# Performance work log

Hardware: AMD Instinct MI355X
Metric: run time of the kernel (lower is better)

The kernel has to match this reference:

```python
import jax, jax.numpy as jnp
import numpy as np

B, L, E, H = 8, 1024, 768, 12
D = E // H  # 64 head dim


def _layernorm(x, scale, bias, eps=1e-6):
    m = jnp.mean(x, axis=-1, keepdims=True)
    v = jnp.var(x, axis=-1, keepdims=True)
    return (x - m) * jax.lax.rsqrt(v + eps) * scale + bias


def setup_inputs() -> dict:
    key = jax.random.key(0)
    ks = jax.random.split(key, 8)
    s = lambda fan_in: 1.0 / np.sqrt(fan_in)  # lecun-normal-ish init scale
    return {
        "x": jax.random.normal(ks[0], (B, L, E), jnp.float32),
        "ln1_scale": jnp.ones((E,), jnp.float32),
        "ln1_bias": jnp.zeros((E,), jnp.float32),
        "w_qkv": jax.random.normal(ks[1], (E, 3 * E), jnp.float32) * s(E),
        "b_qkv": jnp.zeros((3 * E,), jnp.float32),
        "w_proj": jax.random.normal(ks[2], (E, E), jnp.float32) * s(E),
        "b_proj": jnp.zeros((E,), jnp.float32),
        "ln2_scale": jnp.ones((E,), jnp.float32),
        "ln2_bias": jnp.zeros((E,), jnp.float32),
        "w_fc": jax.random.normal(ks[3], (E, 4 * E), jnp.float32) * s(E),
        "b_fc": jnp.zeros((4 * E,), jnp.float32),
        "w_out": jax.random.normal(ks[4], (4 * E, E), jnp.float32) * s(4 * E),
        "b_out": jnp.zeros((E,), jnp.float32),
    }


def reference(x, ln1_scale, ln1_bias, w_qkv, b_qkv, w_proj, b_proj,
              ln2_scale, ln2_bias, w_fc, b_fc, w_out, b_out):
    # eval mode: train=False (all dropouts are identity), mask_len=None
    b, l, _ = x.shape
    # ---- pre-LN causal self-attention ----
    z = _layernorm(x, ln1_scale, ln1_bias)
    qkv = z @ w_qkv + b_qkv                                   # (B, L, 3E)
    # faithful to source: reshape to (B, L, H, 3D) then split last axis
    qkv = qkv.reshape(b, l, H, 3 * D).transpose(0, 2, 1, 3)   # (B, H, L, 3D)
    q, k, v = jnp.split(qkv, 3, axis=-1)                      # each (B, H, L, D)
    attn = jnp.einsum("bhqd,bhkd->bhqk", q, k) / jnp.sqrt(jnp.float32(D))
    mask = jnp.tri(l, dtype=jnp.float32)                      # causal lower-tri
    attn = jnp.where(mask == 0, -1e18, attn)
    attn = jax.nn.softmax(attn, axis=-1)
    y = jnp.einsum("bhqk,bhkd->bhqd", attn, v)                # (B, H, L, D)
    y = y.transpose(0, 2, 1, 3).reshape(b, l, E)
    y = y @ w_proj + b_proj
    x = x + y  # residual (resid dropout is identity in eval)
    # ---- MLP block ----
    z = _layernorm(x, ln2_scale, ln2_bias)
    z = jax.nn.selu(z @ w_fc + b_fc) @ w_out + b_out
    return x + z
```

## Files before the change

kernel.cpp:

```cpp
#include <hip/hip_runtime.h>
#include <hip/hip_bf16.h>

typedef __attribute__((ext_vector_type(8))) short short8;
typedef __attribute__((ext_vector_type(4))) float f32x4;
typedef __attribute__((ext_vector_type(4))) unsigned short us4;

#define AS1 __attribute__((address_space(1)))
#define AS3 __attribute__((address_space(3)))

__device__ __forceinline__ unsigned short f2bf(float f) {
    unsigned u = __float_as_uint(f);
    u += 0x7fffu + ((u >> 16) & 1u);
    return (unsigned short)(u >> 16);
}

__device__ __forceinline__ void gload16(const void* g, void* l) {
    __builtin_amdgcn_global_load_lds((AS1 void*)(g), (AS3 void*)(l), 16, 0, 0);
}

__global__ __launch_bounds__(256) void wT_kernel(const float* __restrict__ in,
                                                 unsigned short* __restrict__ out,
                                                 int K, int N) {
    __shared__ float tile[32][33];
    int tx = threadIdx.x & 31, ty = threadIdx.x >> 5;
    int bn = blockIdx.x * 32, bk = blockIdx.y * 32;
    #pragma unroll
    for (int i = ty; i < 32; i += 8)
        tile[i][tx] = in[(long)(bk + i) * N + bn + tx];
    __syncthreads();
    #pragma unroll
    for (int i = ty; i < 32; i += 8)
        out[(long)(bn + i) * K + bk + tx] = f2bf(tile[tx][i]);
}

__global__ __launch_bounds__(256) void ln_row(const float* __restrict__ x,
                                              const float* __restrict__ sc,
                                              const float* __restrict__ bi,
                                              unsigned short* __restrict__ z) {
    long row = blockIdx.x;
    const float* xr = x + row * 768;
    int t = threadIdx.x;
    float v0 = xr[t], v1 = xr[t + 256], v2 = xr[t + 512];
    float s = v0 + v1 + v2;
    float ss = v0 * v0 + v1 * v1 + v2 * v2;
    #pragma unroll
    for (int m = 1; m < 64; m <<= 1) { s += __shfl_xor(s, m); ss += __shfl_xor(ss, m); }
    __shared__ float red[8];
    int wid = t >> 6;
    if ((t & 63) == 0) { red[wid] = s; red[4 + wid] = ss; }
    __syncthreads();
    s = red[0] + red[1] + red[2] + red[3];
    ss = red[4] + red[5] + red[6] + red[7];
    float mean = s * (1.f / 768.f);
    float var = fmaxf(ss * (1.f / 768.f) - mean * mean, 0.f);
    float rs = rsqrtf(var + 1e-6f);
    unsigned short* zr = z + row * 768;
    zr[t]       = f2bf((v0 - mean) * rs * sc[t]       + bi[t]);
    zr[t + 256] = f2bf((v1 - mean) * rs * sc[t + 256] + bi[t + 256]);
    zr[t + 512] = f2bf((v2 - mean) * rs * sc[t + 512] + bi[t + 512]);
}

template <int MODE>
__global__ __launch_bounds__(256, 2) void gemm_bf16(
    const unsigned short* __restrict__ A, const unsigned short* __restrict__ Bt,
    const float* __restrict__ bias, const float* __restrict__ resid,
    float* __restrict__ outf, unsigned short* __restrict__ outb,
    unsigned short* __restrict__ vt, int M, int N, int K) {
    __shared__ unsigned short As[128 * 64];
    __shared__ unsigned short Bs[128 * 64];
    const int tid = threadIdx.x, lane = tid & 63, wid = tid >> 6;
    const int wr = wid >> 1, wc = wid & 1;
    const long row0 = (long)blockIdx.y * 128, col0 = (long)blockIdx.x * 128;

    f32x4 acc[4][4] = {};
    const int nkt = K >> 6;
    for (int t = 0; t < nkt; ++t) {
        #pragma unroll
        for (int kq = 0; kq < 4; kq++) {
            int U = kq * 256 + tid;
            int r = U >> 3, ch = U & 7;
            int kb = (ch * 16) ^ ((r & 7) << 4);
            gload16(A + (row0 + r) * K + t * 64 + (kb >> 1), &As[(kq * 256 + wid * 64) * 8]);
            gload16(Bt + (col0 + r) * K + t * 64 + (kb >> 1), &Bs[(kq * 256 + wid * 64) * 8]);
        }
        __syncthreads();
        #pragma unroll
        for (int kk = 0; kk < 2; kk++) {
            short8 af[4], bf[4];
            #pragma unroll
            for (int m = 0; m < 4; m++) {
                int r = wr * 64 + m * 16 + (lane & 15);
                int off = r * 128 + ((kk * 64 + ((lane >> 4) * 16)) ^ ((r & 7) << 4));
                af[m] = *(const short8*)((const char*)As + off);
            }
            #pragma unroll
            for (int n = 0; n < 4; n++) {
                int r = wc * 64 + n * 16 + (lane & 15);
                int off = r * 128 + ((kk * 64 + ((lane >> 4) * 16)) ^ ((r & 7) << 4));
                bf[n] = *(const short8*)((const char*)Bs + off);
            }
            #pragma unroll
            for (int m = 0; m < 4; m++)
                #pragma unroll
                for (int n = 0; n < 4; n++)
                    acc[m][n] = __builtin_amdgcn_mfma_f32_16x16x32_bf16(af[m], bf[n], acc[m][n], 0, 0, 0);
        }
        __syncthreads();
    }

    const float LAM = 1.0507009873554805f, LAMAL = 1.7580993408473766f;
    #pragma unroll
    for (int n = 0; n < 4; n++) {
        int c = (int)col0 + wc * 64 + n * 16 + (lane & 15);
        float bv = bias[c];
        #pragma unroll
        for (int m = 0; m < 4; m++) {
            long r0 = row0 + wr * 64 + m * 16 + ((lane >> 4) * 4);
            f32x4 v = acc[m][n];
            v += bv;
            if (MODE == 0) {
                int h = c / 192, rem = c - h * 192;
                if (rem < 128) {
                    #pragma unroll
                    for (int r = 0; r < 4; r++) outb[(r0 + r) * 2304 + c] = f2bf(v[r]);
                } else {
                    int d = rem - 128;
                    long bb = r0 >> 10, l = r0 & 1023;
                    us4 p;
                    #pragma unroll
                    for (int r = 0; r < 4; r++) p[r] = f2bf(v[r]);
                    *(us4*)(vt + ((bb * 12 + h) * 64 + d) * 1024 + l) = p;
                }
            } else if (MODE == 1) {
                #pragma unroll
                for (int r = 0; r < 4; r++)
                    outf[(r0 + r) * (long)N + c] = v[r] + resid[(r0 + r) * (long)N + c];
            } else if (MODE == 2) {
                #pragma unroll
                for (int r = 0; r < 4; r++) {
                    float s = v[r];
                    s = s > 0.f ? LAM * s : LAMAL * (__expf(s) - 1.f);
                    outb[(r0 + r) * (long)N + c] = f2bf(s);
                }
            }
        }
    }
}

__global__ __launch_bounds__(256, 2) void attn_kernel(const unsigned short* __restrict__ qkv,
                                                      const unsigned short* __restrict__ vt,
                                                      unsigned short* __restrict__ y) {
    __shared__ unsigned short Qs[128 * 64];
    __shared__ unsigned short Ks[64 * 64];
    __shared__ unsigned short Vs[64 * 64];
    __shared__ unsigned short Ps[4][32 * 64];
    const int tid = threadIdx.x, lane = tid & 63, wid = tid >> 6;
    const int bh = blockIdx.x, qt = blockIdx.y;
    const int b = bh / 12, h = bh - b * 12;
    const long qrow0 = (long)b * 1024 + qt * 128;

    const unsigned short* qptr = qkv + qrow0 * 2304 + h * 192;
    #pragma unroll
    for (int kq = 0; kq < 4; kq++) {
        int U = kq * 256 + tid;
        int r = U >> 3, ch = U & 7;
        int kb = (ch * 16) ^ ((r & 7) << 4);
        gload16(qptr + (long)r * 2304 + (kb >> 1), &Qs[(kq * 256 + wid * 64) * 8]);
    }
    __syncthreads();
    short8 qf[2][2];
    #pragma unroll
    for (int m = 0; m < 2; m++)
        #pragma unroll
        for (int kk = 0; kk < 2; kk++) {
            int r = wid * 32 + m * 16 + (lane & 15);
            int off = r * 128 + ((kk * 64 + ((lane >> 4) * 16)) ^ ((r & 7) << 4));
            qf[m][kk] = *(const short8*)((const char*)Qs + off);
        }

    f32x4 O[2][4] = {};
    float mrow[2][4], lrow[2][4];
    #pragma unroll
    for (int m = 0; m < 2; m++)
        #pragma unroll
        for (int r = 0; r < 4; r++) { mrow[m][r] = -3.0e38f; lrow[m][r] = 0.f; }

    const int qlo = qt * 128 + wid * 32;
    const int nkv = (qt + 1) * 2;
    const unsigned short* kptr = qkv + (long)b * 1024 * 2304 + h * 192 + 64;
    const unsigned short* vptr = vt + (long)bh * 64 * 1024;

    for (int kvt = 0; kvt < nkv; ++kvt) {
        #pragma unroll
        for (int kq = 0; kq < 2; kq++) {
            int U = kq * 256 + tid;
            int r = U >> 3, ch = U & 7;
            int kb = (ch * 16) ^ ((r & 7) << 4);
            gload16(kptr + (long)(kvt * 64 + r) * 2304 + (kb >> 1), &Ks[(kq * 256 + wid * 64) * 8]);
            gload16(vptr + (long)r * 1024 + kvt * 64 + (kb >> 1), &Vs[(kq * 256 + wid * 64) * 8]);
        }
        __syncthreads();
        if (kvt * 64 <= qlo + 31) {
            f32x4 s[2][4] = {};
            #pragma unroll
            for (int kk = 0; kk < 2; kk++) {
                short8 kf[4];
                #pragma unroll
                for (int n = 0; n < 4; n++) {
                    int r = n * 16 + (lane & 15);
                    int off = r * 128 + ((kk * 64 + ((lane >> 4) * 16)) ^ ((r & 7) << 4));
                    kf[n] = *(const short8*)((const char*)Ks + off);
                }
                #pragma unroll
                for (int m = 0; m < 2; m++)
                    #pragma unroll
                    for (int n = 0; n < 4; n++)
                        s[m][n] = __builtin_amdgcn_mfma_f32_16x16x32_bf16(qf[m][kk], kf[n], s[m][n], 0, 0, 0);
            }
            const bool needmask = (kvt * 64 + 63) > qlo;
            #pragma unroll
            for (int m = 0; m < 2; m++)
                #pragma unroll
                for (int n = 0; n < 4; n++) {
                    s[m][n] = s[m][n] * 0.125f;
                    if (needmask) {
                        int c = kvt * 64 + n * 16 + (lane & 15);
                        #pragma unroll
                        for (int r = 0; r < 4; r++) {
                            int rr = qlo + m * 16 + ((lane >> 4) * 4) + r;
                            if (c > rr) s[m][n][r] = -1.0e30f;
                        }
                    }
                }
            #pragma unroll
            for (int m = 0; m < 2; m++)
                #pragma unroll
                for (int r = 0; r < 4; r++) {
                    float mx = fmaxf(fmaxf(s[m][0][r], s[m][1][r]), fmaxf(s[m][2][r], s[m][3][r]));
                    #pragma unroll
                    for (int msk = 1; msk < 16; msk <<= 1) mx = fmaxf(mx, __shfl_xor(mx, msk));
                    float mnew = fmaxf(mrow[m][r], mx);
                    float al = __expf(mrow[m][r] - mnew);
                    float ps = 0.f;
                    #pragma unroll
                    for (int n = 0; n < 4; n++) {
                        float p = __expf(s[m][n][r] - mnew);
                        s[m][n][r] = p;
                        ps += p;
                    }
                    #pragma unroll
                    for (int msk = 1; msk < 16; msk <<= 1) ps += __shfl_xor(ps, msk);
                    lrow[m][r] = lrow[m][r] * al + ps;
                    mrow[m][r] = mnew;
                    #pragma unroll
                    for (int n = 0; n < 4; n++) O[m][n][r] *= al;
                }
            unsigned short* pw = Ps[wid];
            #pragma unroll
            for (int m = 0; m < 2; m++)
                #pragma unroll
                for (int n = 0; n < 4; n++)
                    #pragma unroll
                    for (int r = 0; r < 4; r++) {
                        int pr = m * 16 + ((lane >> 4) * 4) + r;
                        int off = (pr * 128 + (n * 16 + (lane & 15)) * 2) ^ ((pr & 7) << 4);
                        *(unsigned short*)((char*)pw + off) = f2bf(s[m][n][r]);
                    }
            #pragma unroll
            for (int kk = 0; kk < 2; kk++) {
                short8 pf[2], vf[4];
                #pragma unroll
                for (int m = 0; m < 2; m++) {
                    int r = m * 16 + (lane & 15);
                    int off = r * 128 + ((kk * 64 + ((lane >> 4) * 16)) ^ ((r & 7) << 4));
                    pf[m] = *(const short8*)((const char*)pw + off);
                }
                #pragma unroll
                for (int n = 0; n < 4; n++) {
                    int r = n * 16 + (lane & 15);
                    int off = r * 128 + ((kk * 64 + ((lane >> 4) * 16)) ^ ((r & 7) << 4));
                    vf[n] = *(const short8*)((const char*)Vs + off);
                }
                #pragma unroll
                for (int m = 0; m < 2; m++)
                    #pragma unroll
                    for (int n = 0; n < 4; n++)
                        O[m][n] = __builtin_amdgcn_mfma_f32_16x16x32_bf16(pf[m], vf[n], O[m][n], 0, 0, 0);
            }
        }
        __syncthreads();
    }
    unsigned short* yb = y + (qrow0 + wid * 32) * 768 + h * 64;
    #pragma unroll
    for (int m = 0; m < 2; m++)
        #pragma unroll
        for (int n = 0; n < 4; n++)
            #pragma unroll
            for (int r = 0; r < 4; r++) {
                int rr = m * 16 + ((lane >> 4) * 4) + r;
                yb[(long)rr * 768 + n * 16 + (lane & 15)] = f2bf(O[m][n][r] / lrow[m][r]);
            }
}

extern "C" void kernel_launch(void* const* d_in, const int* in_sizes, int n_in,
                              void* d_out, int out_size, void* d_ws, size_t ws_size,
                              hipStream_t stream) {
    (void)in_sizes; (void)n_in; (void)out_size; (void)ws_size;
    const float* x      = (const float*)d_in[0];
    const float* ln1_s  = (const float*)d_in[1];
    const float* ln1_b  = (const float*)d_in[2];
    const float* w_qkv  = (const float*)d_in[3];
    const float* b_qkv  = (const float*)d_in[4];
    const float* w_proj = (const float*)d_in[5];
    const float* b_proj = (const float*)d_in[6];
    const float* ln2_s  = (const float*)d_in[7];
    const float* ln2_b  = (const float*)d_in[8];
    const float* w_fc   = (const float*)d_in[9];
    const float* b_fc   = (const float*)d_in[10];
    const float* w_out  = (const float*)d_in[11];
    const float* b_out  = (const float*)d_in[12];

    unsigned short* wqkvT = (unsigned short*)d_ws;
    unsigned short* wprojT = wqkvT + (size_t)2304 * 768;
    unsigned short* wfcT   = wprojT + (size_t)768 * 768;
    unsigned short* woutT  = wfcT + (size_t)3072 * 768;
    unsigned short* zbuf   = woutT + (size_t)768 * 3072;
    unsigned short* qkvb   = zbuf + (size_t)8192 * 768;
    unsigned short* vtb    = qkvb + (size_t)8192 * 2304;
    unsigned short* abuf   = qkvb;
    float* x2 = (float*)(vtb + (size_t)96 * 64 * 1024);

    wT_kernel<<<dim3(72, 24), 256, 0, stream>>>(w_qkv, wqkvT, 768, 2304);
    wT_kernel<<<dim3(24, 24), 256, 0, stream>>>(w_proj, wprojT, 768, 768);
    wT_kernel<<<dim3(96, 24), 256, 0, stream>>>(w_fc, wfcT, 768, 3072);
    wT_kernel<<<dim3(24, 96), 256, 0, stream>>>(w_out, woutT, 3072, 768);

    ln_row<<<8192, 256, 0, stream>>>(x, ln1_s, ln1_b, zbuf);
    gemm_bf16<0><<<dim3(18, 64), 256, 0, stream>>>(zbuf, wqkvT, b_qkv, nullptr, nullptr, qkvb, vtb, 8192, 2304, 768);
    attn_kernel<<<dim3(96, 8), 256, 0, stream>>>(qkvb, vtb, zbuf);
    gemm_bf16<1><<<dim3(6, 64), 256, 0, stream>>>(zbuf, wprojT, b_proj, x, x2, nullptr, nullptr, 8192, 768, 768);
    ln_row<<<8192, 256, 0, stream>>>(x2, ln2_s, ln2_b, zbuf);
    gemm_bf16<2><<<dim3(24, 64), 256, 0, stream>>>(zbuf, wfcT, b_fc, nullptr, nullptr, abuf, nullptr, 8192, 3072, 768);
    gemm_bf16<1><<<dim3(6, 64), 256, 0, stream>>>(abuf, woutT, b_out, x2, (float*)d_out, nullptr, nullptr, 8192, 768, 3072);
}
```

Before: 423.2 us.

## Add double-buffered 256x256 GEMM and pair causal attention tiles per block

Adds a 512-thread GEMM kernel with 256x256 tiles that double-buffers LDS, prefetches the next K tile in two halves between MFMA phases, and raises wave priority around MFMA runs. It is used for the QKV and FC projections. The attention kernel now handles two query tiles per block (qt and 7-qt), which evens out the causal work per block and halves the grid. The cost is 128KB of LDS per block and more registers, which may limit occupancy, and a smaller grid for both kernels.

```diff
diff --git a/kernel.cpp b/kernel.cpp
--- a/kernel.cpp
+++ b/kernel.cpp
@@ -7,6 +7,9 @@
 
 #define AS1 __attribute__((address_space(1)))
 #define AS3 __attribute__((address_space(3)))
+
+#define BARRIER() asm volatile("s_barrier" ::: "memory")
+#define WAITV0()  asm volatile("s_waitcnt vmcnt(0)" ::: "memory")
 
 __device__ __forceinline__ unsigned short f2bf(float f) {
     unsigned u = __float_as_uint(f);
@@ -61,6 +64,153 @@
 }
 
 template <int MODE>
+__global__ __launch_bounds__(512, 2) void gemm256(
+    const unsigned short* __restrict__ A, const unsigned short* __restrict__ Bt,
+    const float* __restrict__ bias,
+    float* __restrict__ outf, unsigned short* __restrict__ outb,
+    unsigned short* __restrict__ vt, int M, int N, int K) {
+    __shared__ unsigned short As[2][256 * 64];
+    __shared__ unsigned short Bs[2][256 * 64];
+    const int tid = threadIdx.x, lane = tid & 63, wid = tid >> 6;
+    const int wm = wid >> 2, wn = wid & 3;
+    const long row0 = (long)blockIdx.y * 256, col0 = (long)blockIdx.x * 256;
+    const int nkt = K >> 6;
+
+    auto stgA = [&](int buf, int t, int h) {
+        #pragma unroll
+        for (int j = 0; j < 2; j++) {
+            int U = j * 512 + tid;
+            int r = (U >> 3) + h * 128, ch = U & 7;
+            int kb = (ch * 16) ^ ((r & 7) << 4);
+            gload16(A + (row0 + r) * K + (long)t * 64 + (kb >> 1), &As[buf][(h * 1024 + U) * 8]);
+        }
+    };
+    auto stgB = [&](int buf, int t, int h) {
+        #pragma unroll
+        for (int j = 0; j < 2; j++) {
+            int U = j * 512 + tid;
+            int r = (U >> 3) + h * 128, ch = U & 7;
+            int kb = (ch * 16) ^ ((r & 7) << 4);
+            gload16(Bt + (col0 + r) * K + (long)t * 64 + (kb >> 1), &Bs[buf][(h * 1024 + U) * 8]);
+        }
+    };
+    auto rdA = [&](int buf, int m, int kk) -> short8 {
+        int r = wm * 128 + m * 16 + (lane & 15);
+        int off = r * 128 + ((kk * 64 + ((lane >> 4) * 16)) ^ ((r & 7) << 4));
+        return *(const short8*)((const char*)&As[buf][0] + off);
+    };
+    auto rdB = [&](int buf, int n, int kk) -> short8 {
+        int r = wn * 64 + n * 16 + (lane & 15);
+        int off = r * 128 + ((kk * 64 + ((lane >> 4) * 16)) ^ ((r & 7) << 4));
+        return *(const short8*)((const char*)&Bs[buf][0] + off);
+    };
+
+    f32x4 acc[8][4] = {};
+    stgA(0, 0, 0); stgB(0, 0, 0); stgA(0, 0, 1); stgB(0, 0, 1);
+    WAITV0();
+    BARRIER();
+
+    short8 a4[4][2], bl[2][2], bh[2][2];
+    for (int t = 0; t < nkt; ++t) {
+        const int cur = t & 1, nxt = cur ^ 1;
+        const bool pf = (t + 1 < nkt);
+        if (pf) { stgA(nxt, t + 1, 0); stgB(nxt, t + 1, 0); }
+        #pragma unroll
+        for (int m = 0; m < 4; m++) { a4[m][0] = rdA(cur, m, 0); a4[m][1] = rdA(cur, m, 1); }
+        #pragma unroll
+        for (int n = 0; n < 2; n++) { bl[n][0] = rdB(cur, n, 0); bl[n][1] = rdB(cur, n, 1); }
+        BARRIER();
+        __builtin_amdgcn_s_setprio(1);
+        #pragma unroll
+        for (int m = 0; m < 4; m++)
+            #pragma unroll
+            for (int n = 0; n < 2; n++)
+                #pragma unroll
+                for (int kk = 0; kk < 2; kk++)
+                    acc[m][n] = __builtin_amdgcn_mfma_f32_16x16x32_bf16(a4[m][kk], bl[n][kk], acc[m][n], 0, 0, 0);
+        __builtin_amdgcn_s_setprio(0);
+        BARRIER();
+        if (pf) { stgA(nxt, t + 1, 1); stgB(nxt, t + 1, 1); }
+        #pragma unroll
+        for (int n = 0; n < 2; n++) { bh[n][0] = rdB(cur, n + 2, 0); bh[n][1] = rdB(cur, n + 2, 1); }
+        BARRIER();
+        __builtin_amdgcn_s_setprio(1);
+        #pragma unroll
+        for (int m = 0; m < 4; m++)
+            #pragma unroll
+            for (int n = 0; n < 2; n++)
+                #pragma unroll
+                for (int kk = 0; kk < 2; kk++)
+                    acc[m][n + 2] = __builtin_amdgcn_mfma_f32_16x16x32_bf16(a4[m][kk], bh[n][kk], acc[m][n + 2], 0, 0, 0);
+        __builtin_amdgcn_s_setprio(0);
+        BARRIER();
+        #pragma unroll
+        for (int m = 0; m < 4; m++) { a4[m][0] = rdA(cur, m + 4, 0); a4[m][1] = rdA(cur, m + 4, 1); }
+        BARRIER();
+        __builtin_amdgcn_s_setprio(1);
+        #pragma unroll
+        for (int m = 0; m < 4; m++)
+            #pragma unroll
+            for (int n = 0; n < 2; n++)
+                #pragma unroll
+                for (int kk = 0; kk < 2; kk++)
+                    acc[m + 4][n + 2] = __builtin_amdgcn_mfma_f32_16x16x32_bf16(a4[m][kk], bh[n][kk], acc[m + 4][n + 2], 0, 0, 0);
+        __builtin_amdgcn_s_setprio(0);
+        BARRIER();
+        WAITV0();
+        BARRIER();
+        __builtin_amdgcn_s_setprio(1);
+        #pragma unroll
+        for (int m = 0; m < 4; m++)
+            #pragma unroll
+            for (int n = 0; n < 2; n++)
+                #pragma unroll
+                for (int kk = 0; kk < 2; kk++)
+                    acc[m + 4][n] = __builtin_amdgcn_mfma_f32_16x16x32_bf16(a4[m][kk], bl[n][kk], acc[m + 4][n], 0, 0, 0);
+        __builtin_amdgcn_s_setprio(0);
+        BARRIER();
+    }
+
+    const float LAM = 1.0507009873554805f, LAMAL = 1.7580993408473766f;
+    #pragma unroll
+    for (int n = 0; n < 4; n++) {
+        int c = (int)col0 + wn * 64 + n * 16 + (lane & 15);
+        float bv = bias[c];
+        #pragma unroll
+        for (int m = 0; m < 8; m++) {
+            long r0 = row0 + wm * 128 + m * 16 + ((lane >> 4) * 4);
+            f32x4 v = acc[m][n];
+            v += bv;
+            if (MODE == 0) {
+                int h = c / 192, rem = c - h * 192;
+                if (rem < 128) {
+                    #pragma unroll
+                    for (int r = 0; r < 4; r++) outb[(r0 + r) * 2304 + c] = f2bf(v[r]);
+                } else {
+                    int d = rem - 128;
+                    long bb = r0 >> 10, l = r0 & 1023;
+                    us4 p;
+                    #pragma unroll
+                    for (int r = 0; r < 4; r++) p[r] = f2bf(v[r]);
+                    *(us4*)(vt + ((bb * 12 + h) * 64 + d) * 1024 + l) = p;
+                }
+            } else if (MODE == 2) {
+                #pragma unroll
+                for (int r = 0; r < 4; r++) {
+                    float s = v[r];
+                    s = s > 0.f ? LAM * s : LAMAL * (__expf(s) - 1.f);
+                    outb[(r0 + r) * (long)N + c] = f2bf(s);
+                }
+            } else {
+                #pragma unroll
+                for (int r = 0; r < 4; r++)
+                    outf[(r0 + r) * (long)N + c] = v[r];
+            }
+        }
+    }
+}
+
+template <int MODE>
 __global__ __launch_bounds__(256, 2) void gemm_bf16(
     const unsigned short* __restrict__ A, const unsigned short* __restrict__ Bt,
     const float* __restrict__ bias, const float* __restrict__ resid,
@@ -108,7 +258,6 @@
         __syncthreads();
     }
 
-    const float LAM = 1.0507009873554805f, LAMAL = 1.7580993408473766f;
     #pragma unroll
     for (int n = 0; n < 4; n++) {
         int c = (int)col0 + wc * 64 + n * 16 + (lane & 15);
@@ -118,31 +267,9 @@
             long r0 = row0 + wr * 64 + m * 16 + ((lane >> 4) * 4);
             f32x4 v = acc[m][n];
             v += bv;
-            if (MODE == 0) {
-                int h = c / 192, rem = c - h * 192;
-                if (rem < 128) {
-                    #pragma unroll
-                    for (int r = 0; r < 4; r++) outb[(r0 + r) * 2304 + c] = f2bf(v[r]);
-                } else {
-                    int d = rem - 128;
-                    long bb = r0 >> 10, l = r0 & 1023;
-                    us4 p;
-                    #pragma unroll
-                    for (int r = 0; r < 4; r++) p[r] = f2bf(v[r]);
-                    *(us4*)(vt + ((bb * 12 + h) * 64 + d) * 1024 + l) = p;
-                }
-            } else if (MODE == 1) {
-                #pragma unroll
-                for (int r = 0; r < 4; r++)
-                    outf[(r0 + r) * (long)N + c] = v[r] + resid[(r0 + r) * (long)N + c];
-            } else if (MODE == 2) {
-                #pragma unroll
-                for (int r = 0; r < 4; r++) {
-                    float s = v[r];
-                    s = s > 0.f ? LAM * s : LAMAL * (__expf(s) - 1.f);
-                    outb[(r0 + r) * (long)N + c] = f2bf(s);
-                }
-            }
+            #pragma unroll
+            for (int r = 0; r < 4; r++)
+                outf[(r0 + r) * (long)N + c] = v[r] + resid[(r0 + r) * (long)N + c];
         }
     }
 }
@@ -155,151 +282,156 @@
     __shared__ unsigned short Vs[64 * 64];
     __shared__ unsigned short Ps[4][32 * 64];
     const int tid = threadIdx.x, lane = tid & 63, wid = tid >> 6;
-    const int bh = blockIdx.x, qt = blockIdx.y;
+    const int bh = blockIdx.x;
     const int b = bh / 12, h = bh - b * 12;
-    const long qrow0 = (long)b * 1024 + qt * 128;
-
-    const unsigned short* qptr = qkv + qrow0 * 2304 + h * 192;
-    #pragma unroll
-    for (int kq = 0; kq < 4; kq++) {
-        int U = kq * 256 + tid;
-        int r = U >> 3, ch = U & 7;
-        int kb = (ch * 16) ^ ((r & 7) << 4);
-        gload16(qptr + (long)r * 2304 + (kb >> 1), &Qs[(kq * 256 + wid * 64) * 8]);
-    }
-    __syncthreads();
-    short8 qf[2][2];
-    #pragma unroll
-    for (int m = 0; m < 2; m++)
-        #pragma unroll
-        for (int kk = 0; kk < 2; kk++) {
-            int r = wid * 32 + m * 16 + (lane & 15);
-            int off = r * 128 + ((kk * 64 + ((lane >> 4) * 16)) ^ ((r & 7) << 4));
-            qf[m][kk] = *(const short8*)((const char*)Qs + off);
-        }
-
-    f32x4 O[2][4] = {};
-    float mrow[2][4], lrow[2][4];
-    #pragma unroll
-    for (int m = 0; m < 2; m++)
-        #pragma unroll
-        for (int r = 0; r < 4; r++) { mrow[m][r] = -3.0e38f; lrow[m][r] = 0.f; }
-
-    const int qlo = qt * 128 + wid * 32;
-    const int nkv = (qt + 1) * 2;
     const unsigned short* kptr = qkv + (long)b * 1024 * 2304 + h * 192 + 64;
     const unsigned short* vptr = vt + (long)bh * 64 * 1024;
 
-    for (int kvt = 0; kvt < nkv; ++kvt) {
-        #pragma unroll
-        for (int kq = 0; kq < 2; kq++) {
+    #pragma unroll
+    for (int qi = 0; qi < 2; qi++) {
+        const int qt = qi ? (7 - (int)blockIdx.y) : (int)blockIdx.y;
+        const long qrow0 = (long)b * 1024 + qt * 128;
+
+        const unsigned short* qptr = qkv + qrow0 * 2304 + h * 192;
+        #pragma unroll
+        for (int kq = 0; kq < 4; kq++) {
             int U = kq * 256 + tid;
             int r = U >> 3, ch = U & 7;
             int kb = (ch * 16) ^ ((r & 7) << 4);
-            gload16(kptr + (long)(kvt * 64 + r) * 2304 + (kb >> 1), &Ks[(kq * 256 + wid * 64) * 8]);
-            gload16(vptr + (long)r * 1024 + kvt * 64 + (kb >> 1), &Vs[(kq * 256 + wid * 64) * 8]);
+            gload16(qptr + (long)r * 2304 + (kb >> 1), &Qs[(kq * 256 + wid * 64) * 8]);
         }
         __syncthreads();
-        if (kvt * 64 <= qlo + 31) {
-            f32x4 s[2][4] = {};
+        short8 qf[2][2];
+        #pragma unroll
+        for (int m = 0; m < 2; m++)
             #pragma unroll
             for (int kk = 0; kk < 2; kk++) {
-                short8 kf[4];
-                #pragma unroll
-                for (int n = 0; n < 4; n++) {
-                    int r = n * 16 + (lane & 15);
-                    int off = r * 128 + ((kk * 64 + ((lane >> 4) * 16)) ^ ((r & 7) << 4));
-                    kf[n] = *(const short8*)((const char*)Ks + off);
+                int r = wid * 32 + m * 16 + (lane & 15);
+                int off = r * 128 + ((kk * 64 + ((lane >> 4) * 16)) ^ ((r & 7) << 4));
+                qf[m][kk] = *(const short8*)((const char*)Qs + off);
+            }
+
+        f32x4 O[2][4] = {};
+        float mrow[2][4], lrow[2][4];
+        #pragma unroll
+        for (int m = 0; m < 2; m++)
+            #pragma unroll
+            for (int r = 0; r < 4; r++) { mrow[m][r] = -3.0e38f; lrow[m][r] = 0.f; }
+
+        const int qlo = qt * 128 + wid * 32;
+        const int nkv = (qt + 1) * 2;
+
+        for (int kvt = 0; kvt < nkv; ++kvt) {
+            #pragma unroll
+            for (int kq = 0; kq < 2; kq++) {
+                int U = kq * 256 + tid;
+                int r = U >> 3, ch = U & 7;
+                int kb = (ch * 16) ^ ((r & 7) << 4);
+                gload16(kptr + (long)(kvt * 64 + r) * 2304 + (kb >> 1), &Ks[(kq * 256 + wid * 64) * 8]);
+                gload16(vptr + (long)r * 1024 + kvt * 64 + (kb >> 1), &Vs[(kq * 256 + wid * 64) * 8]);
+            }
+            __syncthreads();
+            if (kvt * 64 <= qlo + 31) {
+                f32x4 s[2][4] = {};
+                #pragma unroll
+                for (int kk = 0; kk < 2; kk++) {
+                    short8 kf[4];
+                    #pragma unroll
+                    for (int n = 0; n < 4; n++) {
+                        int r = n * 16 + (lane & 15);
+                        int off = r * 128 + ((kk * 64 + ((lane >> 4) * 16)) ^ ((r & 7) << 4));
+                        kf[n] = *(const short8*)((const char*)Ks + off);
+                    }
+                    #pragma unroll
+                    for (int m = 0; m < 2; m++)
+                        #pragma unroll
+                        for (int n = 0; n < 4; n++)
+                            s[m][n] = __builtin_amdgcn_mfma_f32_16x16x32_bf16(qf[m][kk], kf[n], s[m][n], 0, 0, 0);
                 }
+                const bool needmask = (kvt * 64 + 63) > qlo;
                 #pragma unroll
                 for (int m = 0; m < 2; m++)
                     #pragma unroll
-                    for (int n = 0; n < 4; n++)
-                        s[m][n] = __builtin_amdgcn_mfma_f32_16x16x32_bf16(qf[m][kk], kf[n], s[m][n], 0, 0, 0);
-            }
-            const bool needmask = (kvt * 64 + 63) > qlo;
-            #pragma unroll
-            for (int m = 0; m < 2; m++)
-                #pragma unroll
-                for (int n = 0; n < 4; n++) {
-                    s[m][n] = s[m][n] * 0.125f;
-                    if (needmask) {
-                        int c = kvt * 64 + n * 16 + (lane & 15);
-                        #pragma unroll
-                        for (int r = 0; r < 4; r++) {
-                            int rr = qlo + m * 16 + ((lane >> 4) * 4) + r;
-                            if (c > rr) s[m][n][r] = -1.0e30f;
+                    for (int n = 0; n < 4; n++) {
+                        s[m][n] = s[m][n] * 0.125f;
+                        if (needmask) {
+                            int c = kvt * 64 + n * 16 + (lane & 15);
+                            #pragma unroll
+                            for (int r = 0; r < 4; r++) {
+                                int rr = qlo + m * 16 + ((lane >> 4) * 4) + r;
+                                if (c > rr) s[m][n][r] = -1.0e30f;
+                            }
                         }
                     }
+                #pragma unroll
+                for (int m = 0; m < 2; m++)
+                    #pragma unroll
+                    for (int r = 0; r < 4; r++) {
+                        float mx = fmaxf(fmaxf(s[m][0][r], s[m][1][r]), fmaxf(s[m][2][r], s[m][3][r]));
+                        #pragma unroll
+                        for (int msk = 1; msk < 16; msk <<= 1) mx = fmaxf(mx, __shfl_xor(mx, msk));
+                        float mnew = fmaxf(mrow[m][r], mx);
+                        float al = __expf(mrow[m][r] - mnew);
+                        float ps = 0.f;
+                        #pragma unroll
+                        for (int n = 0; n < 4; n++) {
+                            float p = __expf(s[m][n][r] - mnew);
+                            s[m][n][r] = p;
+                            ps += p;
+                        }
+                        #pragma unroll
+                        for (int msk = 1; msk < 16; msk <<= 1) ps += __shfl_xor(ps, msk);
+                        lrow[m][r] = lrow[m][r] * al + ps;
+                        mrow[m][r] = mnew;
+                        #pragma unroll
+                        for (int n = 0; n < 4; n++) O[m][n][r] *= al;
+                    }
+                unsigned short* pw = Ps[wid];
+                #pragma unroll
+                for (int m = 0; m < 2; m++)
+                    #pragma unroll
+                    for (int n = 0; n < 4; n++)
+                        #pragma unroll
+                        for (int r = 0; r < 4; r++) {
+                            int pr = m * 16 + ((lane >> 4) * 4) + r;
+                            int off = (pr * 128 + (n * 16 + (lane & 15)) * 2) ^ ((pr & 7) << 4);
+                            *(unsigned short*)((char*)pw + off) = f2bf(s[m][n][r]);
+                        }
+                #pragma unroll
+                for (int kk = 0; kk < 2; kk++) {
+                    short8 pf[2], vf[4];
+                    #pragma unroll
+                    for (int m = 0; m < 2; m++) {
+                        int r = m * 16 + (lane & 15);
+                        int off = r * 128 + ((kk * 64 + ((lane >> 4) * 16)) ^ ((r & 7) << 4));
+                        pf[m] = *(const short8*)((const char*)pw + off);
+                    }
+                    #pragma unroll
+                    for (int n = 0; n < 4; n++) {
+                        int r = n * 16 + (lane & 15);
+                        int off = r * 128 + ((kk * 64 + ((lane >> 4) * 16)) ^ ((r & 7) << 4));
+                        vf[n] = *(const short8*)((const char*)Vs + off);
+                    }
+                    #pragma unroll
+                    for (int m = 0; m < 2; m++)
+                        #pragma unroll
+                        for (int n = 0; n < 4; n++)
+                            O[m][n] = __builtin_amdgcn_mfma_f32_16x16x32_bf16(pf[m], vf[n], O[m][n], 0, 0, 0);
                 }
-            #pragma unroll
-            for (int m = 0; m < 2; m++)
+            }
+            __syncthreads();
+        }
+        unsigned short* yb = y + (qrow0 + wid * 32) * 768 + h * 64;
+        #pragma unroll
+        for (int m = 0; m < 2; m++)
+            #pragma unroll
+            for (int n = 0; n < 4; n++)
                 #pragma unroll
                 for (int r = 0; r < 4; r++) {
-                    float mx = fmaxf(fmaxf(s[m][0][r], s[m][1][r]), fmaxf(s[m][2][r], s[m][3][r]));
-                    #pragma unroll
-                    for (int msk = 1; msk < 16; msk <<= 1) mx = fmaxf(mx, __shfl_xor(mx, msk));
-                    float mnew = fmaxf(mrow[m][r], mx);
-                    float al = __expf(mrow[m][r] - mnew);
-                    float ps = 0.f;
-                    #pragma unroll
-                    for (int n = 0; n < 4; n++) {
-                        float p = __expf(s[m][n][r] - mnew);
-                        s[m][n][r] = p;
-                        ps += p;
-                    }
-                    #pragma unroll
-                    for (int msk = 1; msk < 16; msk <<= 1) ps += __shfl_xor(ps, msk);
-                    lrow[m][r] = lrow[m][r] * al + ps;
-                    mrow[m][r] = mnew;
-                    #pragma unroll
-                    for (int n = 0; n < 4; n++) O[m][n][r] *= al;
+                    int rr = m * 16 + ((lane >> 4) * 4) + r;
+                    yb[(long)rr * 768 + n * 16 + (lane & 15)] = f2bf(O[m][n][r] / lrow[m][r]);
                 }
-            unsigned short* pw = Ps[wid];
-            #pragma unroll
-            for (int m = 0; m < 2; m++)
-                #pragma unroll
-                for (int n = 0; n < 4; n++)
-                    #pragma unroll
-                    for (int r = 0; r < 4; r++) {
-                        int pr = m * 16 + ((lane >> 4) * 4) + r;
-                        int off = (pr * 128 + (n * 16 + (lane & 15)) * 2) ^ ((pr & 7) << 4);
-                        *(unsigned short*)((char*)pw + off) = f2bf(s[m][n][r]);
-                    }
-            #pragma unroll
-            for (int kk = 0; kk < 2; kk++) {
-                short8 pf[2], vf[4];
-                #pragma unroll
-                for (int m = 0; m < 2; m++) {
-                    int r = m * 16 + (lane & 15);
-                    int off = r * 128 + ((kk * 64 + ((lane >> 4) * 16)) ^ ((r & 7) << 4));
-                    pf[m] = *(const short8*)((const char*)pw + off);
-                }
-                #pragma unroll
-                for (int n = 0; n < 4; n++) {
-                    int r = n * 16 + (lane & 15);
-                    int off = r * 128 + ((kk * 64 + ((lane >> 4) * 16)) ^ ((r & 7) << 4));
-                    vf[n] = *(const short8*)((const char*)Vs + off);
-                }
-                #pragma unroll
-                for (int m = 0; m < 2; m++)
-                    #pragma unroll
-                    for (int n = 0; n < 4; n++)
-                        O[m][n] = __builtin_amdgcn_mfma_f32_16x16x32_bf16(pf[m], vf[n], O[m][n], 0, 0, 0);
-            }
-        }
-        __syncthreads();
     }
-    unsigned short* yb = y + (qrow0 + wid * 32) * 768 + h * 64;
-    #pragma unroll
-    for (int m = 0; m < 2; m++)
-        #pragma unroll
-        for (int n = 0; n < 4; n++)
-            #pragma unroll
-            for (int r = 0; r < 4; r++) {
-                int rr = m * 16 + ((lane >> 4) * 4) + r;
-                yb[(long)rr * 768 + n * 16 + (lane & 15)] = f2bf(O[m][n][r] / lrow[m][r]);
-            }
 }
 
 extern "C" void kernel_launch(void* const* d_in, const int* in_sizes, int n_in,
@@ -336,10 +468,10 @@
     wT_kernel<<<dim3(24, 96), 256, 0, stream>>>(w_out, woutT, 3072, 768);
 
     ln_row<<<8192, 256, 0, stream>>>(x, ln1_s, ln1_b, zbuf);
-    gemm_bf16<0><<<dim3(18, 64), 256, 0, stream>>>(zbuf, wqkvT, b_qkv, nullptr, nullptr, qkvb, vtb, 8192, 2304, 768);
-    attn_kernel<<<dim3(96, 8), 256, 0, stream>>>(qkvb, vtb, zbuf);
+    gemm256<0><<<dim3(9, 32), 512, 0, stream>>>(zbuf, wqkvT, b_qkv, nullptr, qkvb, vtb, 8192, 2304, 768);
+    attn_kernel<<<dim3(96, 4), 256, 0, stream>>>(qkvb, vtb, zbuf);
     gemm_bf16<1><<<dim3(6, 64), 256, 0, stream>>>(zbuf, wprojT, b_proj, x, x2, nullptr, nullptr, 8192, 768, 768);
     ln_row<<<8192, 256, 0, stream>>>(x2, ln2_s, ln2_b, zbuf);
-    gemm_bf16<2><<<dim3(24, 64), 256, 0, stream>>>(zbuf, wfcT, b_fc, nullptr, nullptr, abuf, nullptr, 8192, 3072, 768);
+    gemm256<2><<<dim3(12, 32), 512, 0, stream>>>(zbuf, wfcT, b_fc, nullptr, abuf, nullptr, 8192, 3072, 768);
     gemm_bf16<1><<<dim3(6, 64), 256, 0, stream>>>(abuf, woutT, b_out, x2, (float*)d_out, nullptr, nullptr, 8192, 768, 3072);
 }
```

Result: slower. 471.4 us (+11.4%).
